# Kernel tuning notes

Measured on AMD Instinct MI355X. Metric: run time of the kernel, lower is better.

## Reference

```python
import jax, jax.numpy as jnp
import numpy as np

N = 4096      # nodes
IN = 512      # in_features
HEADS = 8
HPH = 8       # n_hidden // n_heads
HID = HEADS * HPH  # 64
CLS = 16      # n_classes
NEG_SLOPE = 0.2
MASK_VAL = -1e9


def setup_inputs() -> dict:
    key = jax.random.key(0)
    ks = jax.random.split(key, 8)
    x = jax.random.normal(ks[0], (N, IN), jnp.float32)
    # sparse-ish adjacency, avg degree ~16, with self loops
    adj = jax.random.bernoulli(ks[1], 16.0 / N, (N, N)) | jnp.eye(N, dtype=bool)
    W1 = jax.random.normal(ks[2], (IN, HEADS, HPH), jnp.float32) * 0.05
    a1l = jax.random.normal(ks[3], (HEADS, HPH), jnp.float32) * 0.05
    a1r = jax.random.normal(ks[4], (HEADS, HPH), jnp.float32) * 0.05
    W2 = jax.random.normal(ks[5], (HID, 1, CLS), jnp.float32) * 0.05
    a2l = jax.random.normal(ks[6], (1, CLS), jnp.float32) * 0.05
    a2r = jax.random.normal(ks[7], (1, CLS), jnp.float32) * 0.05
    return {"x": x, "adj": adj, "W1": W1, "a1l": a1l, "a1r": a1r,
            "W2": W2, "a2l": a2l, "a2r": a2r}


def gat_layer(x, adj, W, al, ar, is_concat):
    # project: [N, H, D]
    g = jnp.einsum('ni,ihd->nhd', x, W)
    # score e[i,j,h] = leaky_relu(a_l . g_i + a_r . g_j)
    sl = jnp.einsum('nhd,hd->nh', g, al)  # [N, H]
    sr = jnp.einsum('nhd,hd->nh', g, ar)  # [N, H]
    e = jax.nn.leaky_relu(sl[:, None, :] + sr[None, :, :], NEG_SLOPE)  # [N, N, H]
    e = jnp.where(adj[:, :, None], e, MASK_VAL)
    a = jax.nn.softmax(e, axis=1)                 # softmax over neighbors j
    out = jnp.einsum('ijh,jhd->ihd', a, g)        # [N, H, D]
    if is_concat:
        return out.reshape(out.shape[0], -1)      # [N, H*D]
    return out.mean(axis=1)                        # [N, D]


def reference(x, adj, W1, a1l, a1r, W2, a2l, a2r):
    # dropout layers are identity in eval mode
    h = gat_layer(x, adj, W1, a1l, a1r, True)   # [N, HID]
    h = jax.nn.elu(h)
    return gat_layer(h, adj, W2, a2l, a2r, False)  # [N, CLS]
```

## Files before the change

kernel.cpp:

```cpp
#include <hip/hip_runtime.h>
#include <hip/hip_bf16.h>

#define N_NODES 4096
#define IN_F 512
#define HEADS 8
#define HPH 8
#define HID 64
#define CLS 16
#define NEG_SLOPE 0.2f
#define MAXD 256

__device__ __forceinline__ float leaky(float x) { return x > 0.f ? x : NEG_SLOPE * x; }

__global__ __launch_bounds__(256, 4) void scan_proj1(
        const int* __restrict__ adj,
        const float* __restrict__ x,
        const float* __restrict__ W1,
        const float* __restrict__ a1l,
        const float* __restrict__ a1r,
        float* __restrict__ g1,
        float* __restrict__ sl1,
        float* __restrict__ sr1,
        int* __restrict__ deg_g,
        int* __restrict__ nbr_g) {
    __shared__ float xs[16][516];
    __shared__ int cntS[4];
    const int b = blockIdx.x;
    const int t = threadIdx.x;
    const int group = b / 5;
    const int role = b - group * 5;
    if (role < 4) {
        int* nbrS = (int*)&xs[0][0];
        const int w = t >> 6, lane = t & 63;
        if (lane == 0) cntS[w] = 0;
        const int i = (group * 4 + role) * 4 + w;
        const int4* row = (const int4*)(adj + (size_t)i * N_NODES);
        int4 v[16];
#pragma unroll
        for (int s = 0; s < 16; ++s) v[s] = row[lane + 64 * s];
#pragma unroll
        for (int s = 0; s < 16; ++s) {
            const int base = 4 * (lane + 64 * s);
            if (v[s].x | v[s].y | v[s].z | v[s].w) {
                if (v[s].x) { int p = atomicAdd(&cntS[w], 1); if (p < MAXD) nbrS[w * MAXD + p] = base; }
                if (v[s].y) { int p = atomicAdd(&cntS[w], 1); if (p < MAXD) nbrS[w * MAXD + p] = base + 1; }
                if (v[s].z) { int p = atomicAdd(&cntS[w], 1); if (p < MAXD) nbrS[w * MAXD + p] = base + 2; }
                if (v[s].w) { int p = atomicAdd(&cntS[w], 1); if (p < MAXD) nbrS[w * MAXD + p] = base + 3; }
            }
        }
        const int n = cntS[w] < MAXD ? cntS[w] : MAXD;
        if (lane == 0) deg_g[i] = n;
        for (int k = lane; k < n; k += 64) nbr_g[(size_t)i * MAXD + k] = nbrS[w * MAXD + k];
        return;
    }
    const int i0 = group * 16;
    for (int l = t; l < 2048; l += 256) {
        const int r = l >> 7, c4 = l & 127;
        *(float4*)&xs[r][c4 * 4] = *(const float4*)(x + (size_t)(i0 + r) * IN_F + c4 * 4);
    }
    __syncthreads();
    const int wv = t >> 6;
    const int inner = t & 63;
    const int kq = inner >> 4;
    const int cg = inner & 15;
    float4 acc[4];
#pragma unroll
    for (int r = 0; r < 4; ++r) acc[r] = make_float4(0.f, 0.f, 0.f, 0.f);
    const float* xr[4];
#pragma unroll
    for (int r = 0; r < 4; ++r) xr[r] = &xs[wv * 4 + r][kq * 128];
    const float* Wq = W1 + (size_t)(kq * 128) * HID + cg * 4;
#pragma unroll 2
    for (int k = 0; k < 128; k += 4) {
        const float4 w0 = *(const float4*)(Wq + (size_t)(k + 0) * HID);
        const float4 w1 = *(const float4*)(Wq + (size_t)(k + 1) * HID);
        const float4 w2 = *(const float4*)(Wq + (size_t)(k + 2) * HID);
        const float4 w3 = *(const float4*)(Wq + (size_t)(k + 3) * HID);
#pragma unroll
        for (int r = 0; r < 4; ++r) {
            const float4 xv = *(const float4*)(xr[r] + k);
            acc[r].x += xv.x * w0.x + xv.y * w1.x + xv.z * w2.x + xv.w * w3.x;
            acc[r].y += xv.x * w0.y + xv.y * w1.y + xv.z * w2.y + xv.w * w3.y;
            acc[r].z += xv.x * w0.z + xv.y * w1.z + xv.z * w2.z + xv.w * w3.z;
            acc[r].w += xv.x * w0.w + xv.y * w1.w + xv.z * w2.w + xv.w * w3.w;
        }
    }
#pragma unroll
    for (int r = 0; r < 4; ++r) {
#pragma unroll
        for (int m = 16; m <= 32; m <<= 1) {
            acc[r].x += __shfl_xor(acc[r].x, m, 64);
            acc[r].y += __shfl_xor(acc[r].y, m, 64);
            acc[r].z += __shfl_xor(acc[r].z, m, 64);
            acc[r].w += __shfl_xor(acc[r].w, m, 64);
        }
    }
    if (kq == 0) {
        const float4 al = *(const float4*)(a1l + cg * 4);
        const float4 ar = *(const float4*)(a1r + cg * 4);
#pragma unroll
        for (int r = 0; r < 4; ++r) {
            const int i = i0 + wv * 4 + r;
            *(float4*)(g1 + (size_t)i * HID + cg * 4) = acc[r];
            float pl = acc[r].x * al.x + acc[r].y * al.y + acc[r].z * al.z + acc[r].w * al.w;
            float pr = acc[r].x * ar.x + acc[r].y * ar.y + acc[r].z * ar.z + acc[r].w * ar.w;
            pl += __shfl_xor(pl, 1, 64);
            pr += __shfl_xor(pr, 1, 64);
            if ((cg & 1) == 0) {
                sl1[i * HEADS + (cg >> 1)] = pl;
                sr1[i * HEADS + (cg >> 1)] = pr;
            }
        }
    }
}

__global__ __launch_bounds__(256) void attn1_fused(
        const float* __restrict__ g1,
        const float* __restrict__ sl1,
        const float* __restrict__ sr1,
        const float* __restrict__ W2,
        const float* __restrict__ a2l,
        const float* __restrict__ a2r,
        const int* __restrict__ deg_g,
        const int* __restrict__ nbr_g,
        float* __restrict__ g2,
        float* __restrict__ sl2,
        float* __restrict__ sr2) {
    __shared__ int nbr[4][MAXD];
    __shared__ float h1s[4][HID];
    const int w = threadIdx.x >> 6;
    const int t = threadIdx.x & 63;
    const int i = blockIdx.x * 4 + w;
    const int n = deg_g[i];
    for (int k = t; k < n; k += 64) nbr[w][k] = nbr_g[(size_t)i * MAXD + k];
    const int h = t >> 3;
    const float sl = sl1[i * HEADS + h];
    float denom = 0.f, acc = 0.f;
    int k = 0;
    for (; k + 4 <= n; k += 4) {
        const int j0 = nbr[w][k], j1 = nbr[w][k + 1], j2 = nbr[w][k + 2], j3 = nbr[w][k + 3];
        const float s0 = sr1[j0 * HEADS + h], s1 = sr1[j1 * HEADS + h];
        const float s2 = sr1[j2 * HEADS + h], s3 = sr1[j3 * HEADS + h];
        const float v0 = g1[(size_t)j0 * HID + t], v1 = g1[(size_t)j1 * HID + t];
        const float v2 = g1[(size_t)j2 * HID + t], v3 = g1[(size_t)j3 * HID + t];
        const float w0 = __expf(leaky(sl + s0)), w1 = __expf(leaky(sl + s1));
        const float w2 = __expf(leaky(sl + s2)), w3 = __expf(leaky(sl + s3));
        denom += (w0 + w1) + (w2 + w3);
        acc += w0 * v0; acc += w1 * v1; acc += w2 * v2; acc += w3 * v3;
    }
    for (; k < n; ++k) {
        const int jj = nbr[w][k];
        const float wq = __expf(leaky(sl + sr1[jj * HEADS + h]));
        denom += wq;
        acc += wq * g1[(size_t)jj * HID + t];
    }
    float o = (n > 0) ? (acc / denom) : 0.f;
    o = (o > 0.f) ? o : expm1f(o);
    h1s[w][t] = o;
    const int q = t >> 4, c = t & 15;
    float p = 0.f;
#pragma unroll
    for (int kk = 0; kk < 16; ++kk) {
        const int k2 = q * 16 + kk;
        p += h1s[w][k2] * W2[k2 * CLS + c];
    }
    p += __shfl_xor(p, 16, 64);
    p += __shfl_xor(p, 32, 64);
    float pl = 0.f, pr = 0.f;
    if (t < CLS) {
        g2[(size_t)i * CLS + t] = p;
        pl = p * a2l[t];
        pr = p * a2r[t];
    }
#pragma unroll
    for (int off = 1; off < 16; off <<= 1) {
        pl += __shfl_xor(pl, off, 64);
        pr += __shfl_xor(pr, off, 64);
    }
    if (t == 0) { sl2[i] = pl; sr2[i] = pr; }
}

__global__ __launch_bounds__(256) void attn2(
        const int* __restrict__ deg_g,
        const int* __restrict__ nbr_g,
        const float* __restrict__ g2,
        const float* __restrict__ sl2,
        const float* __restrict__ sr2,
        float* __restrict__ out) {
    __shared__ int nbrs[16][MAXD];
    const int w = threadIdx.x >> 6;
    const int t = threadIdx.x & 63;
    const int g = t >> 4;
    const int c = t & 15;
    const int node = blockIdx.x * 16 + w * 4 + g;
    int* myn = nbrs[w * 4 + g];
    const int n = deg_g[node];
    for (int k = c; k < n; k += 16) myn[k] = nbr_g[(size_t)node * MAXD + k];
    const float sl = sl2[node];
    float denom = 0.f, acc = 0.f;
    int k = 0;
    for (; k + 4 <= n; k += 4) {
        const int j0 = myn[k], j1 = myn[k + 1];
        const int j2 = myn[k + 2], j3 = myn[k + 3];
        const float s0 = sr2[j0], s1 = sr2[j1], s2 = sr2[j2], s3 = sr2[j3];
        const float v0 = g2[(size_t)j0 * CLS + c], v1 = g2[(size_t)j1 * CLS + c];
        const float v2 = g2[(size_t)j2 * CLS + c], v3 = g2[(size_t)j3 * CLS + c];
        const float w0 = __expf(leaky(sl + s0)), w1 = __expf(leaky(sl + s1));
        const float w2 = __expf(leaky(sl + s2)), w3 = __expf(leaky(sl + s3));
        denom += (w0 + w1) + (w2 + w3);
        acc += w0 * v0; acc += w1 * v1; acc += w2 * v2; acc += w3 * v3;
    }
    for (; k < n; ++k) {
        const int jj = myn[k];
        const float wq = __expf(leaky(sl + sr2[jj]));
        denom += wq;
        acc += wq * g2[(size_t)jj * CLS + c];
    }
    out[(size_t)node * CLS + c] = (n > 0) ? acc / denom : 0.f;
}

extern "C" void kernel_launch(void* const* d_in, const int* in_sizes, int n_in,
                              void* d_out, int out_size, void* d_ws, size_t ws_size,
                              hipStream_t stream) {
    const float* x   = (const float*)d_in[0];
    const int*   adj = (const int*)d_in[1];
    const float* W1  = (const float*)d_in[2];
    const float* a1l = (const float*)d_in[3];
    const float* a1r = (const float*)d_in[4];
    const float* W2  = (const float*)d_in[5];
    const float* a2l = (const float*)d_in[6];
    const float* a2r = (const float*)d_in[7];
    float* out = (float*)d_out;

    float* ws  = (float*)d_ws;
    float* g1  = ws;
    float* sl1 = g1  + (size_t)N_NODES * HID;
    float* sr1 = sl1 + (size_t)N_NODES * HEADS;
    float* g2  = sr1 + (size_t)N_NODES * HEADS;
    float* sl2 = g2  + (size_t)N_NODES * CLS;
    float* sr2 = sl2 + N_NODES;
    int*   deg = (int*)(sr2 + N_NODES);
    int*   nbr = deg + N_NODES;

    scan_proj1<<<5 * (N_NODES / 16), 256, 0, stream>>>(
        adj, x, W1, a1l, a1r, g1, sl1, sr1, deg, nbr);
    attn1_fused<<<N_NODES / 4, 256, 0, stream>>>(g1, sl1, sr1, W2, a2l, a2r,
                                                 deg, nbr, g2, sl2, sr2);
    attn2<<<N_NODES / 16, 256, 0, stream>>>(deg, nbr, g2, sl2, sr2, out);
}
```

Measured before the change: 129.1 us.

## Split adjacency row scan across block with ballot compaction; replace LDS neighbor lists with shuffles

Each adjacency row is now scanned by a whole 256-thread block, with each wave covering one quarter of the row. Neighbors are compacted with ballot/popcount prefix sums instead of per-element LDS atomics, and per-wave offsets are merged through a syncthreads. The attention kernels now hold neighbor indices in registers and broadcast them with shuffles instead of staging them in shared memory, falling back to global loads past 64 neighbors. The aim is more parallelism on the memory-bound adjacency read and less LDS traffic and atomic serialization, at the cost of launching more blocks and running more shuffles.

```diff
diff --git a/kernel.cpp b/kernel.cpp
--- a/kernel.cpp
+++ b/kernel.cpp
@@ -9,6 +9,7 @@
 #define CLS 16
 #define NEG_SLOPE 0.2f
 #define MAXD 256
+#define QCAP 256
 
 __device__ __forceinline__ float leaky(float x) { return x > 0.f ? x : NEG_SLOPE * x; }
 
@@ -24,33 +25,95 @@
         int* __restrict__ deg_g,
         int* __restrict__ nbr_g) {
     __shared__ float xs[16][516];
-    __shared__ int cntS[4];
+    __shared__ int wcnt[4];
     const int b = blockIdx.x;
     const int t = threadIdx.x;
-    const int group = b / 5;
-    const int role = b - group * 5;
-    if (role < 4) {
+    const int group = b / 17;
+    const int role = b - group * 17;
+    if (role < 16) {
         int* nbrS = (int*)&xs[0][0];
         const int w = t >> 6, lane = t & 63;
-        if (lane == 0) cntS[w] = 0;
-        const int i = (group * 4 + role) * 4 + w;
-        const int4* row = (const int4*)(adj + (size_t)i * N_NODES);
-        int4 v[16];
-#pragma unroll
-        for (int s = 0; s < 16; ++s) v[s] = row[lane + 64 * s];
-#pragma unroll
-        for (int s = 0; s < 16; ++s) {
-            const int base = 4 * (lane + 64 * s);
-            if (v[s].x | v[s].y | v[s].z | v[s].w) {
-                if (v[s].x) { int p = atomicAdd(&cntS[w], 1); if (p < MAXD) nbrS[w * MAXD + p] = base; }
-                if (v[s].y) { int p = atomicAdd(&cntS[w], 1); if (p < MAXD) nbrS[w * MAXD + p] = base + 1; }
-                if (v[s].z) { int p = atomicAdd(&cntS[w], 1); if (p < MAXD) nbrS[w * MAXD + p] = base + 2; }
-                if (v[s].w) { int p = atomicAdd(&cntS[w], 1); if (p < MAXD) nbrS[w * MAXD + p] = base + 3; }
-            }
-        }
-        const int n = cntS[w] < MAXD ? cntS[w] : MAXD;
-        if (lane == 0) deg_g[i] = n;
-        for (int k = lane; k < n; k += 64) nbr_g[(size_t)i * MAXD + k] = nbrS[w * MAXD + k];
+        const int i = group * 16 + role;
+        const int4* q = (const int4*)(adj + (size_t)i * N_NODES) + w * 256;
+        const int4 v0 = q[lane];
+        const int4 v1 = q[lane + 64];
+        const int4 v2 = q[lane + 128];
+        const int4 v3 = q[lane + 192];
+        const unsigned long long below = (1ull << lane) - 1ull;
+        int* seg = nbrS + w * QCAP;
+        const int jq = w * 1024;
+        int segcnt = 0;
+        {
+            const int4 v = v0; const int s = 0;
+            const bool fx = v.x != 0, fy = v.y != 0, fz = v.z != 0, fw = v.w != 0;
+            const unsigned long long bx = __ballot(fx), by = __ballot(fy);
+            const unsigned long long bz = __ballot(fz), bw = __ballot(fw);
+            int base = segcnt + __popcll(bx & below) + __popcll(by & below)
+                              + __popcll(bz & below) + __popcll(bw & below);
+            const int j0 = jq + 4 * (lane + 64 * s);
+            int r = 0;
+            if (fx) { if (base + r < QCAP) seg[base + r] = j0;     ++r; }
+            if (fy) { if (base + r < QCAP) seg[base + r] = j0 + 1; ++r; }
+            if (fz) { if (base + r < QCAP) seg[base + r] = j0 + 2; ++r; }
+            if (fw) { if (base + r < QCAP) seg[base + r] = j0 + 3; ++r; }
+            segcnt += __popcll(bx) + __popcll(by) + __popcll(bz) + __popcll(bw);
+        }
+        {
+            const int4 v = v1; const int s = 1;
+            const bool fx = v.x != 0, fy = v.y != 0, fz = v.z != 0, fw = v.w != 0;
+            const unsigned long long bx = __ballot(fx), by = __ballot(fy);
+            const unsigned long long bz = __ballot(fz), bw = __ballot(fw);
+            int base = segcnt + __popcll(bx & below) + __popcll(by & below)
+                              + __popcll(bz & below) + __popcll(bw & below);
+            const int j0 = jq + 4 * (lane + 64 * s);
+            int r = 0;
+            if (fx) { if (base + r < QCAP) seg[base + r] = j0;     ++r; }
+            if (fy) { if (base + r < QCAP) seg[base + r] = j0 + 1; ++r; }
+            if (fz) { if (base + r < QCAP) seg[base + r] = j0 + 2; ++r; }
+            if (fw) { if (base + r < QCAP) seg[base + r] = j0 + 3; ++r; }
+            segcnt += __popcll(bx) + __popcll(by) + __popcll(bz) + __popcll(bw);
+        }
+        {
+            const int4 v = v2; const int s = 2;
+            const bool fx = v.x != 0, fy = v.y != 0, fz = v.z != 0, fw = v.w != 0;
+            const unsigned long long bx = __ballot(fx), by = __ballot(fy);
+            const unsigned long long bz = __ballot(fz), bw = __ballot(fw);
+            int base = segcnt + __popcll(bx & below) + __popcll(by & below)
+                              + __popcll(bz & below) + __popcll(bw & below);
+            const int j0 = jq + 4 * (lane + 64 * s);
+            int r = 0;
+            if (fx) { if (base + r < QCAP) seg[base + r] = j0;     ++r; }
+            if (fy) { if (base + r < QCAP) seg[base + r] = j0 + 1; ++r; }
+            if (fz) { if (base + r < QCAP) seg[base + r] = j0 + 2; ++r; }
+            if (fw) { if (base + r < QCAP) seg[base + r] = j0 + 3; ++r; }
+            segcnt += __popcll(bx) + __popcll(by) + __popcll(bz) + __popcll(bw);
+        }
+        {
+            const int4 v = v3; const int s = 3;
+            const bool fx = v.x != 0, fy = v.y != 0, fz = v.z != 0, fw = v.w != 0;
+            const unsigned long long bx = __ballot(fx), by = __ballot(fy);
+            const unsigned long long bz = __ballot(fz), bw = __ballot(fw);
+            int base = segcnt + __popcll(bx & below) + __popcll(by & below)
+                              + __popcll(bz & below) + __popcll(bw & below);
+            const int j0 = jq + 4 * (lane + 64 * s);
+            int r = 0;
+            if (fx) { if (base + r < QCAP) seg[base + r] = j0;     ++r; }
+            if (fy) { if (base + r < QCAP) seg[base + r] = j0 + 1; ++r; }
+            if (fz) { if (base + r < QCAP) seg[base + r] = j0 + 2; ++r; }
+            if (fw) { if (base + r < QCAP) seg[base + r] = j0 + 3; ++r; }
+            segcnt += __popcll(bx) + __popcll(by) + __popcll(bz) + __popcll(bw);
+        }
+        const int myc = segcnt < QCAP ? segcnt : QCAP;
+        if (lane == 0) wcnt[w] = myc;
+        __syncthreads();
+        const int off = (w > 0 ? wcnt[0] : 0) + (w > 1 ? wcnt[1] : 0)
+                      + (w > 2 ? wcnt[2] : 0);
+        const int total = wcnt[0] + wcnt[1] + wcnt[2] + wcnt[3];
+        if (t == 0) deg_g[i] = total < MAXD ? total : MAXD;
+        for (int k = lane; k < myc; k += 64) {
+            const int pos = off + k;
+            if (pos < MAXD) nbr_g[(size_t)i * MAXD + pos] = seg[k];
+        }
         return;
     }
     const int i0 = group * 16;
@@ -126,19 +189,19 @@
         float* __restrict__ g2,
         float* __restrict__ sl2,
         float* __restrict__ sr2) {
-    __shared__ int nbr[4][MAXD];
-    __shared__ float h1s[4][HID];
     const int w = threadIdx.x >> 6;
     const int t = threadIdx.x & 63;
     const int i = blockIdx.x * 4 + w;
     const int n = deg_g[i];
-    for (int k = t; k < n; k += 64) nbr[w][k] = nbr_g[(size_t)i * MAXD + k];
+    const int jreg = nbr_g[(size_t)i * MAXD + t];
     const int h = t >> 3;
     const float sl = sl1[i * HEADS + h];
     float denom = 0.f, acc = 0.f;
+    const int n64 = n < 64 ? n : 64;
     int k = 0;
-    for (; k + 4 <= n; k += 4) {
-        const int j0 = nbr[w][k], j1 = nbr[w][k + 1], j2 = nbr[w][k + 2], j3 = nbr[w][k + 3];
+    for (; k + 4 <= n64; k += 4) {
+        const int j0 = __shfl(jreg, k),     j1 = __shfl(jreg, k + 1);
+        const int j2 = __shfl(jreg, k + 2), j3 = __shfl(jreg, k + 3);
         const float s0 = sr1[j0 * HEADS + h], s1 = sr1[j1 * HEADS + h];
         const float s2 = sr1[j2 * HEADS + h], s3 = sr1[j3 * HEADS + h];
         const float v0 = g1[(size_t)j0 * HID + t], v1 = g1[(size_t)j1 * HID + t];
@@ -148,21 +211,26 @@
         denom += (w0 + w1) + (w2 + w3);
         acc += w0 * v0; acc += w1 * v1; acc += w2 * v2; acc += w3 * v3;
     }
-    for (; k < n; ++k) {
-        const int jj = nbr[w][k];
+    for (; k < n64; ++k) {
+        const int jj = __shfl(jreg, k);
         const float wq = __expf(leaky(sl + sr1[jj * HEADS + h]));
         denom += wq;
         acc += wq * g1[(size_t)jj * HID + t];
     }
+    for (; k < n; ++k) {
+        const int jj = nbr_g[(size_t)i * MAXD + k];
+        const float wq = __expf(leaky(sl + sr1[jj * HEADS + h]));
+        denom += wq;
+        acc += wq * g1[(size_t)jj * HID + t];
+    }
     float o = (n > 0) ? (acc / denom) : 0.f;
     o = (o > 0.f) ? o : expm1f(o);
-    h1s[w][t] = o;
     const int q = t >> 4, c = t & 15;
     float p = 0.f;
 #pragma unroll
     for (int kk = 0; kk < 16; ++kk) {
         const int k2 = q * 16 + kk;
-        p += h1s[w][k2] * W2[k2 * CLS + c];
+        p += __shfl(o, k2) * W2[k2 * CLS + c];
     }
     p += __shfl_xor(p, 16, 64);
     p += __shfl_xor(p, 32, 64);
@@ -187,21 +255,21 @@
         const float* __restrict__ sl2,
         const float* __restrict__ sr2,
         float* __restrict__ out) {
-    __shared__ int nbrs[16][MAXD];
     const int w = threadIdx.x >> 6;
     const int t = threadIdx.x & 63;
     const int g = t >> 4;
     const int c = t & 15;
     const int node = blockIdx.x * 16 + w * 4 + g;
-    int* myn = nbrs[w * 4 + g];
     const int n = deg_g[node];
-    for (int k = c; k < n; k += 16) myn[k] = nbr_g[(size_t)node * MAXD + k];
+    const int4 jv = *(const int4*)(nbr_g + (size_t)node * MAXD + 4 * c);
     const float sl = sl2[node];
     float denom = 0.f, acc = 0.f;
+    const int n64 = n < 64 ? n : 64;
     int k = 0;
-    for (; k + 4 <= n; k += 4) {
-        const int j0 = myn[k], j1 = myn[k + 1];
-        const int j2 = myn[k + 2], j3 = myn[k + 3];
+    for (; k + 4 <= n64; k += 4) {
+        const int src = k >> 2;
+        const int j0 = __shfl(jv.x, src, 16), j1 = __shfl(jv.y, src, 16);
+        const int j2 = __shfl(jv.z, src, 16), j3 = __shfl(jv.w, src, 16);
         const float s0 = sr2[j0], s1 = sr2[j1], s2 = sr2[j2], s3 = sr2[j3];
         const float v0 = g2[(size_t)j0 * CLS + c], v1 = g2[(size_t)j1 * CLS + c];
         const float v2 = g2[(size_t)j2 * CLS + c], v3 = g2[(size_t)j3 * CLS + c];
@@ -210,8 +278,17 @@
         denom += (w0 + w1) + (w2 + w3);
         acc += w0 * v0; acc += w1 * v1; acc += w2 * v2; acc += w3 * v3;
     }
+    for (; k < n64; ++k) {
+        const int src = k >> 2, cm = k & 3;
+        const int jx = __shfl(jv.x, src, 16), jy = __shfl(jv.y, src, 16);
+        const int jz = __shfl(jv.z, src, 16), jw = __shfl(jv.w, src, 16);
+        const int jj = cm == 0 ? jx : (cm == 1 ? jy : (cm == 2 ? jz : jw));
+        const float wq = __expf(leaky(sl + sr2[jj]));
+        denom += wq;
+        acc += wq * g2[(size_t)jj * CLS + c];
+    }
     for (; k < n; ++k) {
-        const int jj = myn[k];
+        const int jj = nbr_g[(size_t)node * MAXD + k];
         const float wq = __expf(leaky(sl + sr2[jj]));
         denom += wq;
         acc += wq * g2[(size_t)jj * CLS + c];
@@ -242,7 +319,7 @@
     int*   deg = (int*)(sr2 + N_NODES);
     int*   nbr = deg + N_NODES;
 
-    scan_proj1<<<5 * (N_NODES / 16), 256, 0, stream>>>(
+    scan_proj1<<<17 * (N_NODES / 16), 256, 0, stream>>>(
         adj, x, W1, a1l, a1r, g1, sl1, sr1, deg, nbr);
     attn1_fused<<<N_NODES / 4, 256, 0, stream>>>(g1, sl1, sr1, W2, a2l, a2r,
                                                  deg, nbr, g2, sl2, sr2);
```

Result: no change. 131.1 us (+1.5%).
